# Performance work log

Measured on AMD Instinct MI355X. Metric: run time of the kernel, lower is better.

The kernel has to match this reference:

```python
import jax, jax.numpy as jnp
import numpy as np

B, T, H, I, O, L = 8, 8192, 256, 256, 256, 2


def setup_inputs() -> dict:
    key = jax.random.key(0)
    ks = jax.random.split(key, 12)
    s = 1.0 / np.sqrt(H)
    inp = {
        "emb": jax.random.normal(ks[0], (B, T, I), jnp.float32),
        "start": jax.random.randint(ks[1], (B, T), 0, 2) > 0,  # bool reset flags
        "h0": jnp.zeros((L, B, H), jnp.float32),               # per-layer initial carry
        "min_w": jax.random.normal(ks[2], (H, I), jnp.float32) * s,
        "min_b": jnp.zeros((H,), jnp.float32),
        "mout_w": jax.random.normal(ks[3], (O, H), jnp.float32) * s,
        "mout_b": jnp.zeros((O,), jnp.float32),
        "Wf_w": jax.random.normal(ks[4], (L, H, H), jnp.float32) * s,
        "Wf_b": jnp.zeros((L, H), jnp.float32),
        "Wh_w": jax.random.normal(ks[5], (L, H, H), jnp.float32) * s,
        "Wh_b": jnp.zeros((L, H), jnp.float32),
        "Uf_w": jax.random.normal(ks[6], (L, H, H), jnp.float32) * s,
        "Uh_w": jax.random.normal(ks[7], (L, H, H), jnp.float32) * s,
        "ff_w": jax.random.normal(ks[8], (L, H, H), jnp.float32) * s,
        "ff_b": jnp.zeros((L, H), jnp.float32),
    }
    return inp


def reference(emb, start, h0, min_w, min_b, mout_w, mout_b,
              Wf_w, Wf_b, Wh_w, Wh_b, Uf_w, Uh_w, ff_w, ff_b):
    # map_in: [B,T,I] -> [B,T,H]
    x = jnp.einsum('bti,hi->bth', emb, min_w) + min_b
    start_t = start.T  # [T,B]
    h_final = []
    for l in range(L):
        # Precompute input-side projections outside the scan (time-parallel).
        xf = jnp.einsum('bth,oh->bto', x, Wf_w[l]) + Wf_b[l]  # [B,T,H]
        xh = jnp.einsum('bth,oh->bto', x, Wh_w[l]) + Wh_b[l]  # [B,T,H]
        Uf = Uf_w[l]
        Uh = Uh_w[l]

        def step(h, inp):
            xft, xht, st = inp  # [B,H], [B,H], [B]
            # Resettable: zero the carry where a new episode starts.
            h = jnp.where(st[:, None], jnp.zeros_like(h), h)
            f = jax.nn.sigmoid(xft + h @ Uf.T)
            h_hat = jnp.tanh(xht + (f * h) @ Uh.T)
            h_new = (1.0 - f) * h + f * h_hat
            return h_new, h_new

        hT, z = jax.lax.scan(step, h0[l],
                             (xf.transpose(1, 0, 2), xh.transpose(1, 0, 2), start_t))
        h_final.append(hT)
        z = z.transpose(1, 0, 2)  # [B,T,H]
        # per-layer feedforward + leaky_relu (slope 0.01)
        x = jax.nn.leaky_relu(jnp.einsum('bth,oh->bto', z, ff_w[l]) + ff_b[l])
    out = jnp.einsum('bth,oh->bto', x, mout_w) + mout_b  # [B,T,O]
    return out, jnp.stack(h_final)  # ([B,T,O], [L,B,H])
```

## Files before the change

### kernel.cpp

```cpp
#include <hip/hip_runtime.h>
#include <hip/hip_fp16.h>
#include <cstdint>
#include <cstddef>

#define BATCH 8
#define TT 8192
#define HD 256
#define RTOT (BATCH * TT)
#define HC 16
#define NPAIR (TT / (2 * HC))

typedef __attribute__((ext_vector_type(4))) float    f32x4;
typedef __attribute__((ext_vector_type(8))) _Float16 f16x8;
typedef __attribute__((ext_vector_type(4))) _Float16 f16x4;

typedef __attribute__((address_space(1))) const void gvoid_t;
typedef __attribute__((address_space(3))) void lvoid_t;

__device__ __forceinline__ void gl_lds16(const void* g, void* l) {
  __builtin_amdgcn_global_load_lds((gvoid_t*)g, (lvoid_t*)l, 16, 0, 0);
}

__device__ __forceinline__ void ldsbar() {
  asm volatile("s_waitcnt lgkmcnt(0)" ::: "memory");
  __builtin_amdgcn_s_barrier();
  __builtin_amdgcn_sched_barrier(0x7F);
}

__global__ void detect_start_par(const unsigned int* __restrict__ s,
                                 int* __restrict__ bad) {
  const unsigned int w = s[blockIdx.x * blockDim.x + threadIdx.x];
  const unsigned int b0 = w & 255u, b1 = (w >> 8) & 255u,
                     b2 = (w >> 16) & 255u, b3 = (w >> 24) & 255u;
  const int bi = (b1 | b2 | b3) != 0;
  const int bf = (b0 != 0) || (b1 != 0) ||
                 (b2 != 0 && b2 != 0x80u) || (b3 != 0 && b3 != 0x3fu);
  if (__any(bi) && (threadIdx.x & 63) == 0) atomicOr(&bad[0], 1);
  if (__any(bf) && (threadIdx.x & 63) == 0) atomicOr(&bad[1], 1);
}

__global__ void conv_f16(const float* __restrict__ in, _Float16* __restrict__ out,
                         const int n) {
  const int i = (blockIdx.x * blockDim.x + threadIdx.x) * 8;
  if (i + 7 >= n) return;
  const float4 a = *(const float4*)&in[i];
  const float4 b = *(const float4*)&in[i + 4];
  f16x8 v;
  v[0] = (_Float16)a.x; v[1] = (_Float16)a.y; v[2] = (_Float16)a.z; v[3] = (_Float16)a.w;
  v[4] = (_Float16)b.x; v[5] = (_Float16)b.y; v[6] = (_Float16)b.z; v[7] = (_Float16)b.w;
  *(f16x8*)&out[i] = v;
}

__global__ void conv_w8(const float* p0, const float* p1, const float* p2,
                        const float* p3, const float* p4, const float* p5,
                        const float* p6, const float* p7,
                        _Float16* __restrict__ out) {
  const int seg = blockIdx.y;
  const float* p;
  switch (seg) {
    case 0: p = p0; break; case 1: p = p1; break;
    case 2: p = p2; break; case 3: p = p3; break;
    case 4: p = p4; break; case 5: p = p5; break;
    case 6: p = p6; break; default: p = p7; break;
  }
  const int i = (blockIdx.x * blockDim.x + threadIdx.x) * 8;
  const float4 a = *(const float4*)&p[i];
  const float4 b = *(const float4*)&p[i + 4];
  f16x8 v;
  v[0] = (_Float16)a.x; v[1] = (_Float16)a.y; v[2] = (_Float16)a.z; v[3] = (_Float16)a.w;
  v[4] = (_Float16)b.x; v[5] = (_Float16)b.y; v[6] = (_Float16)b.z; v[7] = (_Float16)b.w;
  *(f16x8*)&out[(size_t)seg * 65536 + i] = v;
}

__global__ void swz_w(const float* __restrict__ Uf, const float* __restrict__ Uh,
                      _Float16* __restrict__ outp) {
  const int gid  = blockIdx.x * 256 + threadIdx.x;
  const int lane = gid & 63;
  const int w    = (gid >> 6) & 7;
  const int f    = (gid >> 9) & 15;
  const int mat  = (gid >> 13) & 1;
  const int l    = gid >> 14;
  const int fr = lane & 15, fq = lane >> 4;
  const int tile = f >> 3, kc = f & 7;
  const int nrow = (w * 2 + tile) * 16 + fr;
  const int kb   = kc * 32 + fq * 8;
  const float* src = (mat ? Uh : Uf) + (size_t)l * 65536 + nrow * 256 + kb;
  const float4 a = *(const float4*)src;
  const float4 b = *(const float4*)(src + 4);
  f16x8 v;
  v[0] = (_Float16)a.x; v[1] = (_Float16)a.y; v[2] = (_Float16)a.z; v[3] = (_Float16)a.w;
  v[4] = (_Float16)b.x; v[5] = (_Float16)b.y; v[6] = (_Float16)b.z; v[7] = (_Float16)b.w;
  *(f16x8*)&outp[(size_t)gid * 8] = v;
}

__global__ __launch_bounds__(256, 4) void gemm_h(
    const _Float16* __restrict__ A, const _Float16* __restrict__ W,
    const float* __restrict__ bias, _Float16* __restrict__ C16,
    float* __restrict__ C32, const int act) {
  __shared__ __align__(16) char smem[34816];
  _Float16* EP = (_Float16*)smem;

  const int tid  = threadIdx.x;
  const int wave = tid >> 6, lane = tid & 63;
  const int wm = wave >> 1, wn = wave & 1;
  const int swz  = (blockIdx.x & 7) * 128 + (blockIdx.x >> 3);
  const int bm = (swz >> 1) * 128, bn = (swz & 1) * 128;
  const int lrow  = tid >> 2;
  const int lcol8 = (tid & 3) * 8;
  const int fr = lane & 15;
  const int fq = lane >> 4;

  f32x4 acc[4][4];
#pragma unroll
  for (int i = 0; i < 4; i++)
#pragma unroll
    for (int j = 0; j < 4; j++) acc[i][j] = (f32x4){0.f, 0.f, 0.f, 0.f};

  float bv[4];
#pragma unroll
  for (int ni = 0; ni < 4; ni++) bv[ni] = bias[bn + wn * 64 + ni * 16 + fr];

  auto STAGE = [&](int kk, int bb) {
    const int k0 = kk * 32;
#pragma unroll
    for (int is = 0; is < 2; is++) {
      gl_lds16(&A[(size_t)(bm + is * 64 + lrow) * HD + k0 + lcol8],
               smem + bb * 16384 + wave * 1024 + is * 4096);
      gl_lds16(&W[(size_t)(bn + is * 64 + lrow) * HD + k0 + lcol8],
               smem + bb * 16384 + 8192 + wave * 1024 + is * 4096);
    }
  };

  STAGE(0, 0);
#pragma unroll
  for (int k = 0; k < 8; k++) {
    const int cur = k & 1;
    STAGE(k < 7 ? k + 1 : 7, cur ^ 1);
    asm volatile("s_waitcnt vmcnt(4)" ::: "memory");
    __builtin_amdgcn_s_barrier();
    __builtin_amdgcn_sched_barrier(0);
    asm volatile("" ::: "memory");
    const _Float16* As = (const _Float16*)(smem + cur * 16384);
    const _Float16* Ws = (const _Float16*)(smem + cur * 16384 + 8192);
    f16x8 af[4], bf[4];
#pragma unroll
    for (int mi = 0; mi < 4; mi++)
      af[mi] = *(const f16x8*)(As + (wm * 64 + mi * 16 + fr) * 32 + fq * 8);
#pragma unroll
    for (int ni = 0; ni < 4; ni++)
      bf[ni] = *(const f16x8*)(Ws + (wn * 64 + ni * 16 + fr) * 32 + fq * 8);
#pragma unroll
    for (int mi = 0; mi < 4; mi++)
#pragma unroll
      for (int ni = 0; ni < 4; ni++)
        acc[mi][ni] = __builtin_amdgcn_mfma_f32_16x16x32_f16(af[mi], bf[ni],
                                                             acc[mi][ni], 0, 0, 0);
    asm volatile("s_waitcnt lgkmcnt(0)" ::: "memory");
    __builtin_amdgcn_s_barrier();
    __builtin_amdgcn_sched_barrier(0);
    asm volatile("" ::: "memory");
  }
  __syncthreads();

  if (C32) {
#pragma unroll
    for (int mi = 0; mi < 4; mi++)
#pragma unroll
      for (int ni = 0; ni < 4; ni++)
#pragma unroll
        for (int j = 0; j < 4; j++) {
          float v = acc[mi][ni][j] + bv[ni];
          if (act == 1) v = (v > 0.f) ? v : 0.01f * v;
          C32[(size_t)(bm + wm * 64 + mi * 16 + fq * 4 + j) * HD +
              bn + wn * 64 + ni * 16 + fr] = v;
        }
  } else {
#pragma unroll
    for (int mi = 0; mi < 4; mi++)
#pragma unroll
      for (int ni = 0; ni < 4; ni++)
#pragma unroll
        for (int j = 0; j < 4; j++) {
          float v = acc[mi][ni][j] + bv[ni];
          if (act == 1) v = (v > 0.f) ? v : 0.01f * v;
          EP[(wm * 64 + mi * 16 + fq * 4 + j) * 136 + wn * 64 + ni * 16 + fr] =
              (_Float16)v;
        }
    __syncthreads();
#pragma unroll
    for (int ps = 0; ps < 8; ps++) {
      const int row = ps * 16 + (tid >> 4);
      const f16x8 v = *(const f16x8*)(EP + row * 136 + (tid & 15) * 8);
      *(f16x8*)&C16[(size_t)(bm + row) * HD + bn + (tid & 15) * 8] = v;
    }
  }
}

__global__ __launch_bounds__(256, 2) void gemm_dual(
    const _Float16* __restrict__ A,
    const _Float16* __restrict__ W1, const _Float16* __restrict__ W2,
    const float* __restrict__ b1, const float* __restrict__ b2,
    _Float16* __restrict__ C1, _Float16* __restrict__ C2) {
  __shared__ __align__(16) char smem[49152];
  _Float16* EP = (_Float16*)smem;

  const int tid  = threadIdx.x;
  const int wave = tid >> 6, lane = tid & 63;
  const int wm = wave >> 1, wn = wave & 1;
  const int swz  = (blockIdx.x & 7) * 128 + (blockIdx.x >> 3);
  const int bm = (swz >> 1) * 128, bn = (swz & 1) * 128;
  const int lrow  = tid >> 2;
  const int lcol8 = (tid & 3) * 8;
  const int fr = lane & 15;
  const int fq = lane >> 4;

  f32x4 acc1[4][4], acc2[4][4];
#pragma unroll
  for (int i = 0; i < 4; i++)
#pragma unroll
    for (int j = 0; j < 4; j++) {
      acc1[i][j] = (f32x4){0.f, 0.f, 0.f, 0.f};
      acc2[i][j] = (f32x4){0.f, 0.f, 0.f, 0.f};
    }

  float bv1[4], bv2[4];
#pragma unroll
  for (int ni = 0; ni < 4; ni++) {
    bv1[ni] = b1[bn + wn * 64 + ni * 16 + fr];
    bv2[ni] = b2[bn + wn * 64 + ni * 16 + fr];
  }

  auto STAGE = [&](int kk, int bb) {
    const int k0 = kk * 32;
#pragma unroll
    for (int is = 0; is < 2; is++) {
      gl_lds16(&A[(size_t)(bm + is * 64 + lrow) * HD + k0 + lcol8],
               smem + bb * 24576 + wave * 1024 + is * 4096);
      gl_lds16(&W1[(size_t)(bn + is * 64 + lrow) * HD + k0 + lcol8],
               smem + bb * 24576 + 8192 + wave * 1024 + is * 4096);
      gl_lds16(&W2[(size_t)(bn + is * 64 + lrow) * HD + k0 + lcol8],
               smem + bb * 24576 + 16384 + wave * 1024 + is * 4096);
    }
  };

  STAGE(0, 0);
#pragma unroll
  for (int k = 0; k < 8; k++) {
    const int cur = k & 1;
    STAGE(k < 7 ? k + 1 : 7, cur ^ 1);
    asm volatile("s_waitcnt vmcnt(6)" ::: "memory");
    __builtin_amdgcn_s_barrier();
    __builtin_amdgcn_sched_barrier(0);
    asm volatile("" ::: "memory");
    const _Float16* As  = (const _Float16*)(smem + cur * 24576);
    const _Float16* Ws1 = (const _Float16*)(smem + cur * 24576 + 8192);
    const _Float16* Ws2 = (const _Float16*)(smem + cur * 24576 + 16384);
    f16x8 af[4], bf1[4], bf2[4];
#pragma unroll
    for (int mi = 0; mi < 4; mi++)
      af[mi] = *(const f16x8*)(As + (wm * 64 + mi * 16 + fr) * 32 + fq * 8);
#pragma unroll
    for (int ni = 0; ni < 4; ni++) {
      bf1[ni] = *(const f16x8*)(Ws1 + (wn * 64 + ni * 16 + fr) * 32 + fq * 8);
      bf2[ni] = *(const f16x8*)(Ws2 + (wn * 64 + ni * 16 + fr) * 32 + fq * 8);
    }
#pragma unroll
    for (int mi = 0; mi < 4; mi++)
#pragma unroll
      for (int ni = 0; ni < 4; ni++) {
        acc1[mi][ni] = __builtin_amdgcn_mfma_f32_16x16x32_f16(af[mi], bf1[ni],
                                                              acc1[mi][ni], 0, 0, 0);
        acc2[mi][ni] = __builtin_amdgcn_mfma_f32_16x16x32_f16(af[mi], bf2[ni],
                                                              acc2[mi][ni], 0, 0, 0);
      }
    asm volatile("s_waitcnt lgkmcnt(0)" ::: "memory");
    __builtin_amdgcn_s_barrier();
    __builtin_amdgcn_sched_barrier(0);
    asm volatile("" ::: "memory");
  }

#pragma unroll
  for (int which = 0; which < 2; which++) {
    __syncthreads();
#pragma unroll
    for (int mi = 0; mi < 4; mi++)
#pragma unroll
      for (int ni = 0; ni < 4; ni++)
#pragma unroll
        for (int j = 0; j < 4; j++) {
          const float v = (which == 0 ? acc1[mi][ni][j] + bv1[ni]
                                      : acc2[mi][ni][j] + bv2[ni]);
          EP[(wm * 64 + mi * 16 + fq * 4 + j) * 136 + wn * 64 + ni * 16 + fr] =
              (_Float16)v;
        }
    __syncthreads();
    _Float16* Cd = (which == 0) ? C1 : C2;
#pragma unroll
    for (int ps = 0; ps < 8; ps++) {
      const int row = ps * 16 + (tid >> 4);
      const f16x8 v = *(const f16x8*)(EP + row * 136 + (tid & 15) * 8);
      *(f16x8*)&Cd[(size_t)(bm + row) * HD + bn + (tid & 15) * 8] = v;
    }
  }
}

__global__ __launch_bounds__(512) void scan_mgu(
    const _Float16* __restrict__ xf, const _Float16* __restrict__ xh,
    const void* __restrict__ startp, const int* __restrict__ badf,
    const float* __restrict__ h0l,
    const _Float16* __restrict__ wfrag,
    _Float16* __restrict__ z, float* __restrict__ hfin,
    _Float16* __restrict__ dumpz) {
  const int tid  = threadIdx.x;
  const int wave = tid >> 6;
  const int lane = tid & 63;
  const int fr   = lane & 15;
  const int fq   = lane >> 4;
  const int col  = fr;
  const int b    = col & 7;
  const int grp  = col >> 3;
  const int base = blockIdx.x * (2 * HC);
  const int t0c  = base + grp * HC;
  const int mode = (!badf[0]) ? 1 : (!badf[1] ? 2 : 0);

  __shared__ __align__(16) char hbuf[8192];
  __shared__ __align__(16) char gbuf[8192];
  __shared__ int rb[16];

  _Float16* dp0 = dumpz + ((size_t)blockIdx.x * 512 + tid) * 16;

  auto flag = [&](int bb, int t) -> int {
    const int idx = bb * TT + t;
    if (mode == 1) return ((const int*)startp)[idx] != 0;
    if (mode == 2) return ((const float*)startp)[idx] != 0.0f;
    return ((const uint8_t*)startp)[idx] != 0;
  };
  auto ldfrag = [&](const char* buf, int kc) -> f16x8 {
    int off = kc * 1024 + fq * 256 + fr * 16;
    off ^= ((off >> 8) & 1) << 4;
    return *(const f16x8*)(buf + off);
  };
  auto stfrag = [&](char* buf, int nb, const float4 v) {
    int off = ((nb >> 5) * 1024) + (((nb >> 3) & 3) * 256) + col * 16 + (nb & 7) * 2;
    off ^= ((off >> 8) & 1) << 4;
    f16x4 p;
    p[0] = (_Float16)v.x; p[1] = (_Float16)v.y;
    p[2] = (_Float16)v.z; p[3] = (_Float16)v.w;
    *(f16x4*)(buf + off) = p;
  };

  f16x8 auf[2][8], auh[2][8];
#pragma unroll
  for (int f = 0; f < 16; f++)
    auf[f >> 3][f & 7] =
        *(const f16x8*)&wfrag[((size_t)(f * 512) + wave * 64 + lane) * 8];
#pragma unroll
  for (int f = 0; f < 16; f++)
    auh[f >> 3][f & 7] =
        *(const f16x8*)&wfrag[((size_t)(8192 + f * 512) + wave * 64 + lane) * 8];

  if (tid < 16) rb[tid] = -1;
  __syncthreads();
  {
    const int cg  = tid >> 5;
    const int l32 = tid & 31;
    const int t0g = base + (cg >> 3) * HC;
    const int bg  = cg & 7;
    for (int off = 0;; off += 32) {
      const int st = t0g - off - l32;
      if (st >= 0 && rb[cg] < 0 && flag(bg, st)) atomicMax(&rb[cg], st);
      __syncthreads();
      bool done = true;
#pragma unroll
      for (int c = 0; c < 16; c++) {
        const int tc = base + (c >> 3) * HC;
        if (rb[c] < 0 && tc - off >= 0) done = false;
      }
      if (done) break;
      __syncthreads();
    }
  }
  __syncthreads();

  const int rbc    = rb[col];
  const int startc = max(rbc, 0);
  int Lmax = 0;
#pragma unroll
  for (int c = 0; c < 16; c++) {
    const int tc = base + (c >> 3) * HC;
    const int s  = max(rb[c], 0);
    Lmax = max(Lmax, tc - s);
  }

  const int nb0 = (wave * 2 + 0) * 16 + fq * 4;
  const int nb1 = (wave * 2 + 1) * 16 + fq * 4;

  float4 hinit0 = make_float4(0.f, 0.f, 0.f, 0.f), hinit1 = hinit0;
  if (rbc < 0) {
    hinit0 = *(const float4*)&h0l[b * HD + nb0];
    hinit1 = *(const float4*)&h0l[b * HD + nb1];
  }
  float4 hr0 = hinit0, hr1 = hinit1;
  stfrag(hbuf, nb0, hr0);
  stfrag(hbuf, nb1, hr1);
  __syncthreads();

  int t = t0c - Lmax;
  int tcl = min(max(t, 0), TT - 1);
  f16x4 pxf0 = *(const f16x4*)&xf[((size_t)b * TT + tcl) * HD + nb0];
  f16x4 pxf1 = *(const f16x4*)&xf[((size_t)b * TT + tcl) * HD + nb1];
  f16x4 pxh0 = *(const f16x4*)&xh[((size_t)b * TT + tcl) * HD + nb0];
  f16x4 pxh1 = *(const f16x4*)&xh[((size_t)b * TT + tcl) * HD + nb1];
  int fnext;
  {
    const int ftn = flag(b, min(max(t + 1, 0), TT - 1));
    fnext = (t + 1 < TT) ? ftn : 0;
  }

  for (int i = -Lmax; i < HC; i++) {
    t = t0c + i;
    f32x4 cf0 = {(float)pxf0[0], (float)pxf0[1], (float)pxf0[2], (float)pxf0[3]};
    f32x4 cf1 = {(float)pxf1[0], (float)pxf1[1], (float)pxf1[2], (float)pxf1[3]};
    f32x4 ch0 = {(float)pxh0[0], (float)pxh0[1], (float)pxh0[2], (float)pxh0[3]};
    f32x4 ch1 = {(float)pxh1[0], (float)pxh1[1], (float)pxh1[2], (float)pxh1[3]};

    const int fcur = fnext;
    const int tn = min(max(t + 1, 0), TT - 1);
    pxf0 = *(const f16x4*)&xf[((size_t)b * TT + tn) * HD + nb0];
    pxf1 = *(const f16x4*)&xf[((size_t)b * TT + tn) * HD + nb1];
    pxh0 = *(const f16x4*)&xh[((size_t)b * TT + tn) * HD + nb0];
    pxh1 = *(const f16x4*)&xh[((size_t)b * TT + tn) * HD + nb1];
    {
      const int ftn = flag(b, min(max(t + 2, 0), TT - 1));
      fnext = (t + 2 < TT) ? ftn : 0;
    }

    int stn = 0;
    if (t + 1 <= startc) stn = 2;
    else if (fcur) stn = 1;

#pragma unroll
    for (int kc = 0; kc < 8; kc++) {
      const f16x8 bv = ldfrag(hbuf, kc);
      cf0 = __builtin_amdgcn_mfma_f32_16x16x32_f16(auf[0][kc], bv, cf0, 0, 0, 0);
      cf1 = __builtin_amdgcn_mfma_f32_16x16x32_f16(auf[1][kc], bv, cf1, 0, 0, 0);
    }
    f32x4 fv0, fv1;
    float4 g0, g1;
#pragma unroll
    for (int r = 0; r < 4; r++) {
      const float f0 = 1.f / (1.f + __expf(-cf0[r]));
      const float f1 = 1.f / (1.f + __expf(-cf1[r]));
      fv0[r] = f0; fv1[r] = f1;
      (&g0.x)[r] = f0 * (&hr0.x)[r];
      (&g1.x)[r] = f1 * (&hr1.x)[r];
    }
    stfrag(gbuf, nb0, g0);
    stfrag(gbuf, nb1, g1);
    ldsbar();

#pragma unroll
    for (int kc = 0; kc < 8; kc++) {
      const f16x8 bv = ldfrag(gbuf, kc);
      ch0 = __builtin_amdgcn_mfma_f32_16x16x32_f16(auh[0][kc], bv, ch0, 0, 0, 0);
      ch1 = __builtin_amdgcn_mfma_f32_16x16x32_f16(auh[1][kc], bv, ch1, 0, 0, 0);
    }
    float4 hn0, hn1;
    f16x4 zn0, zn1;
#pragma unroll
    for (int r = 0; r < 4; r++) {
      const float e0 = __expf(2.f * ch0[r]);
      const float e1 = __expf(2.f * ch1[r]);
      const float hh0 = 1.f - 2.f / (e0 + 1.f);
      const float hh1 = 1.f - 2.f / (e1 + 1.f);
      (&hn0.x)[r] = (1.f - fv0[r]) * (&hr0.x)[r] + fv0[r] * hh0;
      (&hn1.x)[r] = (1.f - fv1[r]) * (&hr1.x)[r] + fv1[r] * hh1;
      zn0[r] = (_Float16)(&hn0.x)[r];
      zn1[r] = (_Float16)(&hn1.x)[r];
    }
    {
      const size_t tz = (size_t)b * TT + (size_t)max(t, 0);
      _Float16* zp0 = (i >= 0) ? &z[tz * HD + nb0] : dp0;
      _Float16* zp1 = (i >= 0) ? &z[tz * HD + nb1] : dp0 + 8;
      *(f16x4*)zp0 = zn0;
      *(f16x4*)zp1 = zn1;
    }
    hr0 = (stn == 2) ? hinit0 : (stn == 1 ? make_float4(0.f, 0.f, 0.f, 0.f) : hn0);
    hr1 = (stn == 2) ? hinit1 : (stn == 1 ? make_float4(0.f, 0.f, 0.f, 0.f) : hn1);
    stfrag(hbuf, nb0, hr0);
    stfrag(hbuf, nb1, hr1);
    ldsbar();
  }

  if (t0c + HC == TT) {
    *(float4*)&hfin[b * HD + nb0] = hr0;
    *(float4*)&hfin[b * HD + nb1] = hr1;
  }
}

extern "C" void kernel_launch(void* const* d_in, const int* in_sizes, int n_in,
                              void* d_out, int out_size, void* d_ws, size_t ws_size,
                              hipStream_t stream) {
  const float* emb    = (const float*)d_in[0];
  const void*  startp = d_in[1];
  const float* h0     = (const float*)d_in[2];
  const float* min_w  = (const float*)d_in[3];
  const float* min_b  = (const float*)d_in[4];
  const float* mout_w = (const float*)d_in[5];
  const float* mout_b = (const float*)d_in[6];
  const float* Wf_w   = (const float*)d_in[7];
  const float* Wf_b   = (const float*)d_in[8];
  const float* Wh_w   = (const float*)d_in[9];
  const float* Wh_b   = (const float*)d_in[10];
  const float* Uf_w   = (const float*)d_in[11];
  const float* Uh_w   = (const float*)d_in[12];
  const float* ff_w   = (const float*)d_in[13];
  const float* ff_b   = (const float*)d_in[14];

  float* out = (float*)d_out;
  char*  ws  = (char*)d_ws;
  int*   bad = (int*)ws;
  _Float16* w16  = (_Float16*)(ws + 1024);
  _Float16* uswz = (_Float16*)(ws + 1024 + 1048576);
  _Float16* dump = (_Float16*)(ws + 1024 + 1048576 + 524288);
  _Float16* bufE = (_Float16*)(ws + 1024 + 1048576 + 524288 + 4194304);
  _Float16* bufA = bufE + (size_t)RTOT * HD;
  _Float16* bufB = bufA + (size_t)RTOT * HD;
  _Float16* bufC = bufB + (size_t)RTOT * HD;
  float* hfin = out + (size_t)RTOT * HD;
  const size_t WO = (size_t)HD * HD;

  _Float16* w_min = w16;
  _Float16* w_out = w16 + 1 * WO;
  _Float16* w_f0  = w16 + 2 * WO;
  _Float16* w_f1  = w16 + 3 * WO;
  _Float16* w_h0  = w16 + 4 * WO;
  _Float16* w_h1  = w16 + 5 * WO;
  _Float16* w_ff0 = w16 + 6 * WO;
  _Float16* w_ff1 = w16 + 7 * WO;

  hipMemsetAsync(bad, 0, 16, stream);
  detect_start_par<<<64, 256, 0, stream>>>((const unsigned int*)startp, bad);
  conv_f16<<<RTOT * HD / 2048, 256, 0, stream>>>(emb, bufE, RTOT * HD);
  conv_w8<<<dim3(32, 8), 256, 0, stream>>>(min_w, mout_w, Wf_w, Wf_w + WO,
                                           Wh_w, Wh_w + WO, ff_w, ff_w + WO, w16);
  swz_w<<<128, 256, 0, stream>>>(Uf_w, Uh_w, uswz);

  gemm_h<<<1024, 256, 0, stream>>>(bufE, w_min, min_b, bufA, nullptr, 0);
  gemm_dual<<<1024, 256, 0, stream>>>(bufA, w_f0, w_h0, Wf_b, Wh_b, bufB, bufC);
  scan_mgu<<<NPAIR, 512, 0, stream>>>(bufB, bufC, startp, bad, h0,
                                      uswz, bufA, hfin, dump);
  gemm_h<<<1024, 256, 0, stream>>>(bufA, w_ff0, ff_b, bufB, nullptr, 1);
  gemm_dual<<<1024, 256, 0, stream>>>(bufB, w_f1, w_h1, Wf_b + HD, Wh_b + HD, bufC, bufA);
  scan_mgu<<<NPAIR, 512, 0, stream>>>(bufC, bufA, startp, bad, h0 + BATCH * HD,
                                      uswz + (size_t)16384 * 8, bufB, hfin + BATCH * HD, dump);
  gemm_h<<<1024, 256, 0, stream>>>(bufB, w_ff1, ff_b + HD, bufA, nullptr, 1);
  gemm_h<<<1024, 256, 0, stream>>>(bufA, w_out, mout_b, nullptr, out, 0);
}
```

Measured before the change: 357.3 us.

## Fuse back-to-back GEMMs into one kernel keeping intermediate tile in LDS

Replaces the separate gemm_h and gemm_dual launches with a gemm_fused kernel. Each block takes 64 rows, computes the first GEMM (with optional leaky ReLU) into a full-width 64x256 fp16 tile in LDS, then runs one or two second GEMMs from that tile. This drops the global round trip of the intermediate activations (map_in output and ff outputs) and cuts the kernel launches from 7 GEMMs to 3. In exchange the tiles are smaller, so each block reloads the weights more often, LDS use per block goes up, and the wave-level work per tile shrinks.

```diff
diff --git a/kernel.cpp b/kernel.cpp
--- a/kernel.cpp
+++ b/kernel.cpp
@@ -9,6 +9,7 @@
 #define RTOT (BATCH * TT)
 #define HC 16
 #define NPAIR (TT / (2 * HC))
+#define MSTR 272
 
 typedef __attribute__((ext_vector_type(4))) float    f32x4;
 typedef __attribute__((ext_vector_type(8))) _Float16 f16x8;
@@ -25,6 +26,12 @@
   asm volatile("s_waitcnt lgkmcnt(0)" ::: "memory");
   __builtin_amdgcn_s_barrier();
   __builtin_amdgcn_sched_barrier(0x7F);
+}
+
+__device__ __forceinline__ void gbar() {
+  __builtin_amdgcn_s_barrier();
+  __builtin_amdgcn_sched_barrier(0);
+  asm volatile("" ::: "memory");
 }
 
 __global__ void detect_start_par(const unsigned int* __restrict__ s,
@@ -93,213 +100,172 @@
   *(f16x8*)&outp[(size_t)gid * 8] = v;
 }
 
-__global__ __launch_bounds__(256, 4) void gemm_h(
-    const _Float16* __restrict__ A, const _Float16* __restrict__ W,
-    const float* __restrict__ bias, _Float16* __restrict__ C16,
-    float* __restrict__ C32, const int act) {
-  __shared__ __align__(16) char smem[34816];
-  _Float16* EP = (_Float16*)smem;
+__global__ __launch_bounds__(256, 2) void gemm_fused(
+    const _Float16* __restrict__ A,
+    const _Float16* __restrict__ W1, const float* __restrict__ b1, const int act1,
+    const _Float16* __restrict__ Wa, const float* __restrict__ ba,
+    const _Float16* __restrict__ Wb, const float* __restrict__ bb,
+    _Float16* __restrict__ Ca, _Float16* __restrict__ Cb,
+    float* __restrict__ C32) {
+  __shared__ __align__(16) char smem[59392];
+  _Float16* mid = (_Float16*)smem;
+  char* stg = smem + 34816;
+  _Float16* EP = (_Float16*)stg;
 
   const int tid  = threadIdx.x;
   const int wave = tid >> 6, lane = tid & 63;
   const int wm = wave >> 1, wn = wave & 1;
-  const int swz  = (blockIdx.x & 7) * 128 + (blockIdx.x >> 3);
-  const int bm = (swz >> 1) * 128, bn = (swz & 1) * 128;
+  const int bm = blockIdx.x * 64;
   const int lrow  = tid >> 2;
   const int lcol8 = (tid & 3) * 8;
   const int fr = lane & 15;
   const int fq = lane >> 4;
 
-  f32x4 acc[4][4];
-#pragma unroll
-  for (int i = 0; i < 4; i++)
-#pragma unroll
-    for (int j = 0; j < 4; j++) acc[i][j] = (f32x4){0.f, 0.f, 0.f, 0.f};
-
-  float bv[4];
-#pragma unroll
-  for (int ni = 0; ni < 4; ni++) bv[ni] = bias[bn + wn * 64 + ni * 16 + fr];
-
-  auto STAGE = [&](int kk, int bb) {
-    const int k0 = kk * 32;
-#pragma unroll
-    for (int is = 0; is < 2; is++) {
-      gl_lds16(&A[(size_t)(bm + is * 64 + lrow) * HD + k0 + lcol8],
-               smem + bb * 16384 + wave * 1024 + is * 4096);
-      gl_lds16(&W[(size_t)(bn + is * 64 + lrow) * HD + k0 + lcol8],
-               smem + bb * 16384 + 8192 + wave * 1024 + is * 4096);
-    }
-  };
-
-  STAGE(0, 0);
-#pragma unroll
-  for (int k = 0; k < 8; k++) {
-    const int cur = k & 1;
-    STAGE(k < 7 ? k + 1 : 7, cur ^ 1);
-    asm volatile("s_waitcnt vmcnt(4)" ::: "memory");
-    __builtin_amdgcn_s_barrier();
-    __builtin_amdgcn_sched_barrier(0);
-    asm volatile("" ::: "memory");
-    const _Float16* As = (const _Float16*)(smem + cur * 16384);
-    const _Float16* Ws = (const _Float16*)(smem + cur * 16384 + 8192);
-    f16x8 af[4], bf[4];
-#pragma unroll
-    for (int mi = 0; mi < 4; mi++)
-      af[mi] = *(const f16x8*)(As + (wm * 64 + mi * 16 + fr) * 32 + fq * 8);
+  for (int nh = 0; nh < 2; nh++) {
+    f32x4 acc[2][4];
+#pragma unroll
+    for (int i = 0; i < 2; i++)
+#pragma unroll
+      for (int j = 0; j < 4; j++) acc[i][j] = (f32x4){0.f, 0.f, 0.f, 0.f};
+    float bv[4];
 #pragma unroll
     for (int ni = 0; ni < 4; ni++)
-      bf[ni] = *(const f16x8*)(Ws + (wn * 64 + ni * 16 + fr) * 32 + fq * 8);
-#pragma unroll
-    for (int mi = 0; mi < 4; mi++)
+      bv[ni] = b1[nh * 128 + wn * 64 + ni * 16 + fr];
+
+    auto STA = [&](int kk, int bb2) {
+      const int k0 = kk * 32;
+      gl_lds16(&A[(size_t)(bm + lrow) * HD + k0 + lcol8],
+               stg + bb2 * 12288 + wave * 1024);
+#pragma unroll
+      for (int is = 0; is < 2; is++)
+        gl_lds16(&W1[(size_t)(nh * 128 + is * 64 + lrow) * HD + k0 + lcol8],
+                 stg + bb2 * 12288 + 4096 + is * 4096 + wave * 1024);
+    };
+
+    STA(0, 0);
+#pragma unroll
+    for (int k = 0; k < 8; k++) {
+      const int cur = k & 1;
+      STA(k < 7 ? k + 1 : 7, cur ^ 1);
+      asm volatile("s_waitcnt vmcnt(3)" ::: "memory");
+      gbar();
+      const _Float16* As = (const _Float16*)(stg + cur * 12288);
+      const _Float16* Ws = (const _Float16*)(stg + cur * 12288 + 4096);
+      f16x8 af[2], bf[4];
+#pragma unroll
+      for (int mi = 0; mi < 2; mi++)
+        af[mi] = *(const f16x8*)(As + (wm * 32 + mi * 16 + fr) * 32 + fq * 8);
 #pragma unroll
       for (int ni = 0; ni < 4; ni++)
-        acc[mi][ni] = __builtin_amdgcn_mfma_f32_16x16x32_f16(af[mi], bf[ni],
-                                                             acc[mi][ni], 0, 0, 0);
-    asm volatile("s_waitcnt lgkmcnt(0)" ::: "memory");
-    __builtin_amdgcn_s_barrier();
-    __builtin_amdgcn_sched_barrier(0);
-    asm volatile("" ::: "memory");
-  }
-  __syncthreads();
-
-  if (C32) {
-#pragma unroll
-    for (int mi = 0; mi < 4; mi++)
+        bf[ni] = *(const f16x8*)(Ws + (wn * 64 + ni * 16 + fr) * 32 + fq * 8);
+#pragma unroll
+      for (int mi = 0; mi < 2; mi++)
+#pragma unroll
+        for (int ni = 0; ni < 4; ni++)
+          acc[mi][ni] = __builtin_amdgcn_mfma_f32_16x16x32_f16(af[mi], bf[ni],
+                                                               acc[mi][ni], 0, 0, 0);
+      asm volatile("s_waitcnt lgkmcnt(0)" ::: "memory");
+      gbar();
+    }
+    __syncthreads();
+#pragma unroll
+    for (int mi = 0; mi < 2; mi++)
 #pragma unroll
       for (int ni = 0; ni < 4; ni++)
 #pragma unroll
         for (int j = 0; j < 4; j++) {
           float v = acc[mi][ni][j] + bv[ni];
-          if (act == 1) v = (v > 0.f) ? v : 0.01f * v;
-          C32[(size_t)(bm + wm * 64 + mi * 16 + fq * 4 + j) * HD +
-              bn + wn * 64 + ni * 16 + fr] = v;
+          if (act1 == 1) v = (v > 0.f) ? v : 0.01f * v;
+          mid[(wm * 32 + mi * 16 + fq * 4 + j) * MSTR +
+              nh * 128 + wn * 64 + ni * 16 + fr] = (_Float16)v;
         }
-  } else {
-#pragma unroll
-    for (int mi = 0; mi < 4; mi++)
+  }
+  __syncthreads();
+
+  const int nmat = (Wb != nullptr) ? 2 : 1;
+  for (int mat = 0; mat < nmat; mat++) {
+    const _Float16* W2 = mat ? Wb : Wa;
+    const float* b2p   = mat ? bb : ba;
+    _Float16* C16      = mat ? Cb : Ca;
+    for (int nh = 0; nh < 2; nh++) {
+      f32x4 acc[2][4];
+#pragma unroll
+      for (int i = 0; i < 2; i++)
+#pragma unroll
+        for (int j = 0; j < 4; j++) acc[i][j] = (f32x4){0.f, 0.f, 0.f, 0.f};
+      float bv[4];
 #pragma unroll
       for (int ni = 0; ni < 4; ni++)
-#pragma unroll
-        for (int j = 0; j < 4; j++) {
-          float v = acc[mi][ni][j] + bv[ni];
-          if (act == 1) v = (v > 0.f) ? v : 0.01f * v;
-          EP[(wm * 64 + mi * 16 + fq * 4 + j) * 136 + wn * 64 + ni * 16 + fr] =
-              (_Float16)v;
+        bv[ni] = b2p[nh * 128 + wn * 64 + ni * 16 + fr];
+
+      auto STB = [&](int kk, int bb2) {
+        const int k0 = kk * 32;
+#pragma unroll
+        for (int is = 0; is < 2; is++)
+          gl_lds16(&W2[(size_t)(nh * 128 + is * 64 + lrow) * HD + k0 + lcol8],
+                   stg + bb2 * 12288 + is * 4096 + wave * 1024);
+      };
+
+      STB(0, 0);
+#pragma unroll
+      for (int k = 0; k < 8; k++) {
+        const int cur = k & 1;
+        STB(k < 7 ? k + 1 : 7, cur ^ 1);
+        asm volatile("s_waitcnt vmcnt(2)" ::: "memory");
+        gbar();
+        const _Float16* Ws = (const _Float16*)(stg + cur * 12288);
+        f16x8 af[2], bf[4];
+#pragma unroll
+        for (int mi = 0; mi < 2; mi++)
+          af[mi] = *(const f16x8*)(mid + (wm * 32 + mi * 16 + fr) * MSTR +
+                                   k * 32 + fq * 8);
+#pragma unroll
+        for (int ni = 0; ni < 4; ni++)
+          bf[ni] = *(const f16x8*)(Ws + (wn * 64 + ni * 16 + fr) * 32 + fq * 8);
+#pragma unroll
+        for (int mi = 0; mi < 2; mi++)
+#pragma unroll
+          for (int ni = 0; ni < 4; ni++)
+            acc[mi][ni] = __builtin_amdgcn_mfma_f32_16x16x32_f16(af[mi], bf[ni],
+                                                                 acc[mi][ni], 0, 0, 0);
+        asm volatile("s_waitcnt lgkmcnt(0)" ::: "memory");
+        gbar();
+      }
+      __syncthreads();
+
+      if (C32 != nullptr) {
+#pragma unroll
+        for (int mi = 0; mi < 2; mi++)
+#pragma unroll
+          for (int ni = 0; ni < 4; ni++)
+#pragma unroll
+            for (int j = 0; j < 4; j++) {
+              const float v = acc[mi][ni][j] + bv[ni];
+              C32[(size_t)(bm + wm * 32 + mi * 16 + fq * 4 + j) * HD +
+                  nh * 128 + wn * 64 + ni * 16 + fr] = v;
+            }
+        __syncthreads();
+      } else {
+#pragma unroll
+        for (int mi = 0; mi < 2; mi++)
+#pragma unroll
+          for (int ni = 0; ni < 4; ni++)
+#pragma unroll
+            for (int j = 0; j < 4; j++) {
+              const float v = acc[mi][ni][j] + bv[ni];
+              EP[(wm * 32 + mi * 16 + fq * 4 + j) * 136 +
+                 wn * 64 + ni * 16 + fr] = (_Float16)v;
+            }
+        __syncthreads();
+#pragma unroll
+        for (int it = 0; it < 4; it++) {
+          const int unit = it * 256 + tid;
+          const int row = unit >> 4, cg = unit & 15;
+          *(f16x8*)&C16[(size_t)(bm + row) * HD + nh * 128 + cg * 8] =
+              *(const f16x8*)(EP + row * 136 + cg * 8);
         }
-    __syncthreads();
-#pragma unroll
-    for (int ps = 0; ps < 8; ps++) {
-      const int row = ps * 16 + (tid >> 4);
-      const f16x8 v = *(const f16x8*)(EP + row * 136 + (tid & 15) * 8);
-      *(f16x8*)&C16[(size_t)(bm + row) * HD + bn + (tid & 15) * 8] = v;
-    }
-  }
-}
-
-__global__ __launch_bounds__(256, 2) void gemm_dual(
-    const _Float16* __restrict__ A,
-    const _Float16* __restrict__ W1, const _Float16* __restrict__ W2,
-    const float* __restrict__ b1, const float* __restrict__ b2,
-    _Float16* __restrict__ C1, _Float16* __restrict__ C2) {
-  __shared__ __align__(16) char smem[49152];
-  _Float16* EP = (_Float16*)smem;
-
-  const int tid  = threadIdx.x;
-  const int wave = tid >> 6, lane = tid & 63;
-  const int wm = wave >> 1, wn = wave & 1;
-  const int swz  = (blockIdx.x & 7) * 128 + (blockIdx.x >> 3);
-  const int bm = (swz >> 1) * 128, bn = (swz & 1) * 128;
-  const int lrow  = tid >> 2;
-  const int lcol8 = (tid & 3) * 8;
-  const int fr = lane & 15;
-  const int fq = lane >> 4;
-
-  f32x4 acc1[4][4], acc2[4][4];
-#pragma unroll
-  for (int i = 0; i < 4; i++)
-#pragma unroll
-    for (int j = 0; j < 4; j++) {
-      acc1[i][j] = (f32x4){0.f, 0.f, 0.f, 0.f};
-      acc2[i][j] = (f32x4){0.f, 0.f, 0.f, 0.f};
-    }
-
-  float bv1[4], bv2[4];
-#pragma unroll
-  for (int ni = 0; ni < 4; ni++) {
-    bv1[ni] = b1[bn + wn * 64 + ni * 16 + fr];
-    bv2[ni] = b2[bn + wn * 64 + ni * 16 + fr];
-  }
-
-  auto STAGE = [&](int kk, int bb) {
-    const int k0 = kk * 32;
-#pragma unroll
-    for (int is = 0; is < 2; is++) {
-      gl_lds16(&A[(size_t)(bm + is * 64 + lrow) * HD + k0 + lcol8],
-               smem + bb * 24576 + wave * 1024 + is * 4096);
-      gl_lds16(&W1[(size_t)(bn + is * 64 + lrow) * HD + k0 + lcol8],
-               smem + bb * 24576 + 8192 + wave * 1024 + is * 4096);
-      gl_lds16(&W2[(size_t)(bn + is * 64 + lrow) * HD + k0 + lcol8],
-               smem + bb * 24576 + 16384 + wave * 1024 + is * 4096);
-    }
-  };
-
-  STAGE(0, 0);
-#pragma unroll
-  for (int k = 0; k < 8; k++) {
-    const int cur = k & 1;
-    STAGE(k < 7 ? k + 1 : 7, cur ^ 1);
-    asm volatile("s_waitcnt vmcnt(6)" ::: "memory");
-    __builtin_amdgcn_s_barrier();
-    __builtin_amdgcn_sched_barrier(0);
-    asm volatile("" ::: "memory");
-    const _Float16* As  = (const _Float16*)(smem + cur * 24576);
-    const _Float16* Ws1 = (const _Float16*)(smem + cur * 24576 + 8192);
-    const _Float16* Ws2 = (const _Float16*)(smem + cur * 24576 + 16384);
-    f16x8 af[4], bf1[4], bf2[4];
-#pragma unroll
-    for (int mi = 0; mi < 4; mi++)
-      af[mi] = *(const f16x8*)(As + (wm * 64 + mi * 16 + fr) * 32 + fq * 8);
-#pragma unroll
-    for (int ni = 0; ni < 4; ni++) {
-      bf1[ni] = *(const f16x8*)(Ws1 + (wn * 64 + ni * 16 + fr) * 32 + fq * 8);
-      bf2[ni] = *(const f16x8*)(Ws2 + (wn * 64 + ni * 16 + fr) * 32 + fq * 8);
-    }
-#pragma unroll
-    for (int mi = 0; mi < 4; mi++)
-#pragma unroll
-      for (int ni = 0; ni < 4; ni++) {
-        acc1[mi][ni] = __builtin_amdgcn_mfma_f32_16x16x32_f16(af[mi], bf1[ni],
-                                                              acc1[mi][ni], 0, 0, 0);
-        acc2[mi][ni] = __builtin_amdgcn_mfma_f32_16x16x32_f16(af[mi], bf2[ni],
-                                                              acc2[mi][ni], 0, 0, 0);
+        __syncthreads();
       }
-    asm volatile("s_waitcnt lgkmcnt(0)" ::: "memory");
-    __builtin_amdgcn_s_barrier();
-    __builtin_amdgcn_sched_barrier(0);
-    asm volatile("" ::: "memory");
-  }
-
-#pragma unroll
-  for (int which = 0; which < 2; which++) {
-    __syncthreads();
-#pragma unroll
-    for (int mi = 0; mi < 4; mi++)
-#pragma unroll
-      for (int ni = 0; ni < 4; ni++)
-#pragma unroll
-        for (int j = 0; j < 4; j++) {
-          const float v = (which == 0 ? acc1[mi][ni][j] + bv1[ni]
-                                      : acc2[mi][ni][j] + bv2[ni]);
-          EP[(wm * 64 + mi * 16 + fq * 4 + j) * 136 + wn * 64 + ni * 16 + fr] =
-              (_Float16)v;
-        }
-    __syncthreads();
-    _Float16* Cd = (which == 0) ? C1 : C2;
-#pragma unroll
-    for (int ps = 0; ps < 8; ps++) {
-      const int row = ps * 16 + (tid >> 4);
-      const f16x8 v = *(const f16x8*)(EP + row * 136 + (tid & 15) * 8);
-      *(f16x8*)&Cd[(size_t)(bm + row) * HD + bn + (tid & 15) * 8] = v;
     }
   }
 }
@@ -546,14 +512,18 @@
                                            Wh_w, Wh_w + WO, ff_w, ff_w + WO, w16);
   swz_w<<<128, 256, 0, stream>>>(Uf_w, Uh_w, uswz);
 
-  gemm_h<<<1024, 256, 0, stream>>>(bufE, w_min, min_b, bufA, nullptr, 0);
-  gemm_dual<<<1024, 256, 0, stream>>>(bufA, w_f0, w_h0, Wf_b, Wh_b, bufB, bufC);
+  gemm_fused<<<RTOT / 64, 256, 0, stream>>>(bufE, w_min, min_b, 0,
+                                            w_f0, Wf_b, w_h0, Wh_b,
+                                            bufB, bufC, nullptr);
   scan_mgu<<<NPAIR, 512, 0, stream>>>(bufB, bufC, startp, bad, h0,
                                       uswz, bufA, hfin, dump);
-  gemm_h<<<1024, 256, 0, stream>>>(bufA, w_ff0, ff_b, bufB, nullptr, 1);
-  gemm_dual<<<1024, 256, 0, stream>>>(bufB, w_f1, w_h1, Wf_b + HD, Wh_b + HD, bufC, bufA);
-  scan_mgu<<<NPAIR, 512, 0, stream>>>(bufC, bufA, startp, bad, h0 + BATCH * HD,
-                                      uswz + (size_t)16384 * 8, bufB, hfin + BATCH * HD, dump);
-  gemm_h<<<1024, 256, 0, stream>>>(bufB, w_ff1, ff_b + HD, bufA, nullptr, 1);
-  gemm_h<<<1024, 256, 0, stream>>>(bufA, w_out, mout_b, nullptr, out, 0);
-}
+  gemm_fused<<<RTOT / 64, 256, 0, stream>>>(bufA, w_ff0, ff_b, 1,
+                                            w_f1, Wf_b + HD, w_h1, Wh_b + HD,
+                                            bufB, bufC, nullptr);
+  scan_mgu<<<NPAIR, 512, 0, stream>>>(bufB, bufC, startp, bad, h0 + BATCH * HD,
+                                      uswz + (size_t)16384 * 8, bufA,
+                                      hfin + BATCH * HD, dump);
+  gemm_fused<<<RTOT / 64, 256, 0, stream>>>(bufA, w_ff1, ff_b + HD, 1,
+                                            w_out, mout_b, nullptr, nullptr,
+                                            nullptr, nullptr, out);
+}
```

Result: faster. 350.2 us (-2.0%).
